# Performance work log

Hardware: AMD Instinct MI355X
Metric: run time of the kernel (lower is better)

The kernel has to match this reference:

```python
import jax, jax.numpy as jnp
import numpy as np

HIDDEN = 1024
HEADS = 16
HEAD_DIM = HIDDEN // HEADS


def setup_inputs() -> dict:
    key = jax.random.key(0)
    ks = jax.random.split(key, 4)
    B, S, H = 2, 2048, HIDDEN
    scale = 1.0 / np.sqrt(H)
    return {
        "inputs": jax.random.normal(ks[0], (B, S, H), dtype=jnp.float32),
        "mask": jnp.ones((B, S), dtype=jnp.int32),
        "Wq": jax.random.normal(ks[1], (H, H), dtype=jnp.float32) * scale,
        "bq": jnp.zeros((H,), dtype=jnp.float32),
        "Wk": jax.random.normal(ks[2], (H, H), dtype=jnp.float32) * scale,
        "bk": jnp.zeros((H,), dtype=jnp.float32),
        "Wv": jax.random.normal(ks[3], (H, H), dtype=jnp.float32) * scale,
        "bv": jnp.zeros((H,), dtype=jnp.float32),
    }


def _split_heads(x, B, S):
    # [B,S,H] -> [B,heads,S,head_dim]
    return x.reshape(B, S, HEADS, HEAD_DIM).transpose(0, 2, 1, 3)


def reference(inputs, mask, Wq, bq, Wk, bk, Wv, bv):
    B, S, H = inputs.shape
    q = _split_heads(inputs @ Wq.T + bq, B, S)
    k = _split_heads(inputs @ Wk.T + bk, B, S)
    v = _split_heads(inputs @ Wv.T + bv, B, S)
    scores = jnp.einsum("bhqd,bhkd->bhqk", q, k) / jnp.sqrt(
        jnp.asarray(HEAD_DIM, dtype=inputs.dtype))
    # mask broadcast [B,1,1,S]; zeros -> -inf
    scores = jnp.where(mask[:, None, None, :] == 0, -jnp.inf, scores)
    attn = jax.nn.softmax(scores, axis=-1)
    context = jnp.einsum("bhqk,bhkd->bhqd", attn, v)
    return context.transpose(0, 2, 1, 3).reshape(B, S, H)
```

## Files before the change

kernel.cpp:

```cpp
#include <hip/hip_runtime.h>
#include <hip/hip_fp16.h>

constexpr int S_LEN  = 2048;
constexpr int HID    = 1024;
constexpr int HEADS  = 16;
constexpr int HDIM   = 64;
constexpr int BATCH  = 2;
constexpr int BH     = BATCH * HEADS;
constexpr int M_ROWS = BATCH * S_LEN;

typedef _Float16 half8  __attribute__((ext_vector_type(8)));
typedef _Float16 half4v __attribute__((ext_vector_type(4)));
typedef _Float16 half2v __attribute__((ext_vector_type(2)));
typedef float    f32x4  __attribute__((ext_vector_type(4)));
typedef float    f32x16 __attribute__((ext_vector_type(16)));

constexpr float EXP2_OFF = -11.541560327111707f;
constexpr float Q_SCALE  = 0.18033688011112042f;

__global__ __launch_bounds__(256) void cvt_kernel(
    const float* __restrict__ X,  const float* __restrict__ Wq,
    const float* __restrict__ Wk, const float* __restrict__ Wv,
    const int* __restrict__ mask,
    _Float16* __restrict__ Xh,  _Float16* __restrict__ Wqh,
    _Float16* __restrict__ Wkh, _Float16* __restrict__ Wvh,
    float* __restrict__ maskF)
{
    const int blk = blockIdx.x;
    if (blk >= 3584) {
        const int loc = blk - 3584;
        const size_t e = ((size_t)loc * 256 + threadIdx.x) * 8;
        #pragma unroll
        for (int i = 0; i < 8; ++i)
            maskF[e + i] = mask[e + i] ? EXP2_OFF : -1.0e30f;
        return;
    }
    const float* src; _Float16* dst; int loc;
    if (blk < 2048)      { src = X;  dst = Xh;  loc = blk; }
    else if (blk < 2560) { src = Wq; dst = Wqh; loc = blk - 2048; }
    else if (blk < 3072) { src = Wk; dst = Wkh; loc = blk - 2560; }
    else                 { src = Wv; dst = Wvh; loc = blk - 3072; }
    const size_t e = ((size_t)loc * 256 + threadIdx.x) * 8;
    float4 a = *reinterpret_cast<const float4*>(&src[e]);
    float4 b = *reinterpret_cast<const float4*>(&src[e + 4]);
    half8 h = { (_Float16)a.x, (_Float16)a.y, (_Float16)a.z, (_Float16)a.w,
                (_Float16)b.x, (_Float16)b.y, (_Float16)b.z, (_Float16)b.w };
    *reinterpret_cast<half8*>(&dst[e]) = h;
}

__device__ __forceinline__ void async_cp16(_Float16* lds, const _Float16* g) {
    __builtin_amdgcn_global_load_lds(
        (const __attribute__((address_space(1))) void*)g,
        (__attribute__((address_space(3))) void*)lds, 16, 0, 0);
}

__global__ __launch_bounds__(256) void qkv_proj_kernel(
    const _Float16* __restrict__ Xh,
    const _Float16* __restrict__ Wqh, const _Float16* __restrict__ Wkh,
    const _Float16* __restrict__ Wvh,
    const float* __restrict__ bq, const float* __restrict__ bk,
    const float* __restrict__ bv,
    _Float16* __restrict__ Qo, _Float16* __restrict__ Ko,
    _Float16* __restrict__ Vt)
{
    const int mode = blockIdx.z;
    const _Float16* W    = (mode == 0) ? Wqh : (mode == 1) ? Wkh : Wvh;
    const float*    bias = (mode == 0) ? bq  : (mode == 1) ? bk  : bv;

    const int m0 = blockIdx.x * 128, n0 = blockIdx.y * 128;
    const int tid = threadIdx.x, wave = tid >> 6, lane = tid & 63;
    const int l31 = lane & 31, kg = lane >> 5;

    __shared__ _Float16 SMEM[18432];

    f32x16 acc[2][2];
    #pragma unroll
    for (int mt = 0; mt < 2; ++mt)
        #pragma unroll
        for (int nt = 0; nt < 2; ++nt)
            #pragma unroll
            for (int i = 0; i < 16; ++i) acc[mt][nt][i] = 0.f;

    const int wm = (wave & 1) * 64, wn = (wave >> 1) * 64;

    const int srow = tid >> 2, spos = tid & 3;
    auto stage = [&](int k0, int b) {
        _Float16* Asb = SMEM + b * 8192;
        _Float16* Bsb = Asb + 4096;
        #pragma unroll
        for (int j = 0; j < 2; ++j) {
            const int row = srow + j * 64;
            const int sch = spos ^ (row & 3);
            async_cp16(&Asb[j * 2048 + tid * 8],
                       &Xh[(size_t)(m0 + row) * HID + k0 + sch * 8]);
            async_cp16(&Bsb[j * 2048 + tid * 8],
                       &W [(size_t)(n0 + row) * HID + k0 + sch * 8]);
        }
    };

    stage(0, 0);
    int buf = 0;

    for (int k0 = 0; k0 < HID; k0 += 32) {
        __syncthreads();
        if (k0 + 32 < HID) stage(k0 + 32, buf ^ 1);
        _Float16* Asb = SMEM + buf * 8192;
        _Float16* Bsb = Asb + 4096;

        #pragma unroll
        for (int c = 0; c < 2; ++c) {
            const int k8 = c * 2 + kg;
            half8 af[2], bf[2];
            #pragma unroll
            for (int mt = 0; mt < 2; ++mt) {
                const int row = wm + mt * 32 + l31;
                af[mt] = *reinterpret_cast<const half8*>(
                    &Asb[row * 32 + ((k8 ^ (row & 3)) * 8)]);
            }
            #pragma unroll
            for (int nt = 0; nt < 2; ++nt) {
                const int row = wn + nt * 32 + l31;
                bf[nt] = *reinterpret_cast<const half8*>(
                    &Bsb[row * 32 + ((k8 ^ (row & 3)) * 8)]);
            }
            #pragma unroll
            for (int mt = 0; mt < 2; ++mt)
                #pragma unroll
                for (int nt = 0; nt < 2; ++nt)
                    acc[mt][nt] = __builtin_amdgcn_mfma_f32_32x32x16_f16(
                        af[mt], bf[nt], acc[mt][nt], 0, 0, 0);
        }
        buf ^= 1;
    }
    __syncthreads();

    _Float16* T = SMEM + wave * 4608;

    const int nn  = n0 + wn;
    const int hh  = nn >> 6;
    const int mm  = m0 + wm;
    const int bb  = mm >> 11;
    const int bhv = bb * HEADS + hh;
    const int s0  = mm & 2047;
    const int rowg = lane >> 3, chunk = lane & 7;

    if (mode < 2) {
        _Float16* Out = (mode == 0) ? Qo : Ko;
        #pragma unroll
        for (int nt = 0; nt < 2; ++nt) {
            const int col = nt * 32 + l31;
            float bias_n = bias[nn + col];
            #pragma unroll
            for (int mt = 0; mt < 2; ++mt)
                #pragma unroll
                for (int r = 0; r < 16; ++r) {
                    const int row_l = (r & 3) + 8 * (r >> 2) + 4 * kg;
                    float v = acc[mt][nt][r] + bias_n;
                    if (mode == 0) v *= Q_SCALE;
                    T[(mt * 32 + row_l) * 72 + col] = (_Float16)v;
                }
        }
        asm volatile("s_waitcnt lgkmcnt(0)" ::: "memory");
        #pragma unroll
        for (int j = 0; j < 8; ++j) {
            const int sr = j * 8 + rowg;
            half8 v = *reinterpret_cast<const half8*>(&T[sr * 72 + chunk * 8]);
            *reinterpret_cast<half8*>(
                &Out[((size_t)bhv * S_LEN + s0 + sr) * HDIM + chunk * 8]) = v;
        }
    } else {
        #pragma unroll
        for (int nt = 0; nt < 2; ++nt) {
            const int col = nt * 32 + l31;
            const float bias_n = bias[nn + col];
            #pragma unroll
            for (int mt = 0; mt < 2; ++mt)
                #pragma unroll
                for (int rg = 0; rg < 4; ++rg) {
                    half4v t = { (_Float16)(acc[mt][nt][rg * 4 + 0] + bias_n),
                                 (_Float16)(acc[mt][nt][rg * 4 + 1] + bias_n),
                                 (_Float16)(acc[mt][nt][rg * 4 + 2] + bias_n),
                                 (_Float16)(acc[mt][nt][rg * 4 + 3] + bias_n) };
                    const int s_off = mt * 32 + 8 * rg + 4 * kg;
                    *reinterpret_cast<half4v*>(&T[col * 72 + s_off]) = t;
                }
        }
        asm volatile("s_waitcnt lgkmcnt(0)" ::: "memory");
        #pragma unroll
        for (int j = 0; j < 8; ++j) {
            const int dr = j * 8 + rowg;
            half8 v = *reinterpret_cast<const half8*>(&T[dr * 72 + chunk * 8]);
            *reinterpret_cast<half8*>(
                &Vt[((size_t)bhv * HDIM + dr) * S_LEN + s0 + chunk * 8]) = v;
        }
    }
}

__global__ __launch_bounds__(512) void attn_kernel(
    const _Float16* __restrict__ Q, const _Float16* __restrict__ K,
    const _Float16* __restrict__ Vt, const float* __restrict__ maskF,
    float* __restrict__ Out)
{
    const int id    = blockIdx.x;
    const int xcd   = id & 7, local = id >> 3;
    const int bh    = xcd * 4 + (local & 3);
    const int qt    = local >> 2;
    const int b = bh >> 4, h = bh & 15;
    const int tid = threadIdx.x, wave = tid >> 6, lane = tid & 63;
    const int l15 = lane & 15, quad = lane >> 4;

    __shared__ _Float16 Ks[2][64 * 64];
    __shared__ _Float16 Vs[2][64 * 64];
    __shared__ _Float16 Ps[8][16][68];

    const _Float16* Qb = Q  + (size_t)bh * S_LEN * HDIM;
    const _Float16* Kb = K  + (size_t)bh * S_LEN * HDIM;
    const _Float16* Vb = Vt + (size_t)bh * HDIM * S_LEN;
    const float*    mb = maskF + b * S_LEN;

    const int qrow = qt * 128 + wave * 16 + l15;
    half8 qf[2];
    qf[0] = *reinterpret_cast<const half8*>(&Qb[(size_t)qrow * HDIM + quad * 8]);
    qf[1] = *reinterpret_cast<const half8*>(&Qb[(size_t)qrow * HDIM + 32 + quad * 8]);

    f32x4 acc[4];
    #pragma unroll
    for (int mt = 0; mt < 4; ++mt) acc[mt] = (f32x4){0.f, 0.f, 0.f, 0.f};
    float den = 0.f;

    const int srow_t  = tid >> 3;
    const int schunk  = (tid & 7) ^ (srow_t & 7);
    auto stage = [&](int kb, int buf) {
        async_cp16(&Ks[buf][tid * 8],
                   &Kb[(size_t)(kb + srow_t) * HDIM + schunk * 8]);
        async_cp16(&Vs[buf][tid * 8],
                   &Vb[(size_t)srow_t * S_LEN + kb + schunk * 8]);
    };

    stage(0, 0);
    int buf = 0;
    const int rsw = (l15 & 7);

    for (int kb = 0; kb < S_LEN; kb += 64) {
        __syncthreads();
        if (kb + 64 < S_LEN) stage(kb + 64, buf ^ 1);

        float4 m4[4];
        #pragma unroll
        for (int nt = 0; nt < 4; ++nt)
            m4[nt] = *reinterpret_cast<const float4*>(&mb[kb + nt * 16 + quad * 4]);

        half8 kf[2][4];
        #pragma unroll
        for (int c = 0; c < 2; ++c)
            #pragma unroll
            for (int nt = 0; nt < 4; ++nt)
                kf[c][nt] = *reinterpret_cast<const half8*>(
                    &Ks[buf][(nt * 16 + l15) * 64 + ((c * 4 + quad) ^ rsw) * 8]);
        f32x4 sc[4];
        #pragma unroll
        for (int nt = 0; nt < 4; ++nt) sc[nt] = (f32x4){0.f, 0.f, 0.f, 0.f};
        #pragma unroll
        for (int c = 0; c < 2; ++c)
            #pragma unroll
            for (int nt = 0; nt < 4; ++nt)
                sc[nt] = __builtin_amdgcn_mfma_f32_16x16x32_f16(
                    kf[c][nt], qf[c], sc[nt], 0, 0, 0);

        half8 vf[2][4];
        #pragma unroll
        for (int c = 0; c < 2; ++c)
            #pragma unroll
            for (int mt = 0; mt < 4; ++mt)
                vf[c][mt] = *reinterpret_cast<const half8*>(
                    &Vs[buf][(mt * 16 + l15) * 64 + ((c * 4 + quad) ^ rsw) * 8]);

        #pragma unroll
        for (int nt = 0; nt < 4; ++nt) {
            float p0 = __builtin_amdgcn_exp2f(sc[nt][0] + m4[nt].x);
            float p1 = __builtin_amdgcn_exp2f(sc[nt][1] + m4[nt].y);
            float p2 = __builtin_amdgcn_exp2f(sc[nt][2] + m4[nt].z);
            float p3 = __builtin_amdgcn_exp2f(sc[nt][3] + m4[nt].w);
            den += (p0 + p1) + (p2 + p3);
            half2v lo = __builtin_bit_cast(half2v, __builtin_amdgcn_cvt_pkrtz(p0, p1));
            half2v hi = __builtin_bit_cast(half2v, __builtin_amdgcn_cvt_pkrtz(p2, p3));
            half4v pk = { lo[0], lo[1], hi[0], hi[1] };
            *reinterpret_cast<half4v*>(&Ps[wave][l15][nt * 16 + quad * 4]) = pk;
        }
        asm volatile("s_waitcnt lgkmcnt(0)" ::: "memory");

        #pragma unroll
        for (int c = 0; c < 2; ++c) {
            half4v plo = *reinterpret_cast<const half4v*>(
                &Ps[wave][l15][c * 32 + quad * 8]);
            half4v phi = *reinterpret_cast<const half4v*>(
                &Ps[wave][l15][c * 32 + quad * 8 + 4]);
            half8 pf = { plo[0], plo[1], plo[2], plo[3],
                         phi[0], phi[1], phi[2], phi[3] };
            #pragma unroll
            for (int mt = 0; mt < 4; ++mt)
                acc[mt] = __builtin_amdgcn_mfma_f32_16x16x32_f16(
                    vf[c][mt], pf, acc[mt], 0, 0, 0);
        }
        buf ^= 1;
    }

    den += __shfl_xor(den, 16, 64);
    den += __shfl_xor(den, 32, 64);
    const float inv = 1.0f / den;

    float* orow = Out + ((size_t)(b * S_LEN + qrow)) * HID + h * HDIM;
    #pragma unroll
    for (int mt = 0; mt < 4; ++mt) {
        float4 o = { acc[mt][0] * inv, acc[mt][1] * inv,
                     acc[mt][2] * inv, acc[mt][3] * inv };
        *reinterpret_cast<float4*>(&orow[mt * 16 + quad * 4]) = o;
    }
}

extern "C" void kernel_launch(void* const* d_in, const int* in_sizes, int n_in,
                              void* d_out, int out_size, void* d_ws, size_t ws_size,
                              hipStream_t stream) {
    const float* X  = (const float*)d_in[0];
    const int*   mk = (const int*)  d_in[1];
    const float* Wq = (const float*)d_in[2];
    const float* bq = (const float*)d_in[3];
    const float* Wk = (const float*)d_in[4];
    const float* bk = (const float*)d_in[5];
    const float* Wv = (const float*)d_in[6];
    const float* bv = (const float*)d_in[7];
    float* out = (float*)d_out;

    _Float16* Xh  = (_Float16*)d_ws;
    _Float16* Wqh = Xh  + (size_t)M_ROWS * HID;
    _Float16* Wkh = Wqh + (size_t)HID * HID;
    _Float16* Wvh = Wkh + (size_t)HID * HID;
    _Float16* Q   = Wvh + (size_t)HID * HID;
    _Float16* K   = Q   + (size_t)BH * S_LEN * HDIM;
    _Float16* Vt  = K   + (size_t)BH * S_LEN * HDIM;
    float*    maskF = (float*)(Vt + (size_t)BH * S_LEN * HDIM);

    cvt_kernel<<<3586, 256, 0, stream>>>(X, Wq, Wk, Wv, mk, Xh, Wqh, Wkh, Wvh, maskF);

    dim3 gp(M_ROWS / 128, HID / 128, 3);
    qkv_proj_kernel<<<gp, 256, 0, stream>>>(Xh, Wqh, Wkh, Wvh, bq, bk, bv, Q, K, Vt);

    attn_kernel<<<512, 512, 0, stream>>>(Q, K, Vt, maskF, out);
}
```

Measured before the change: 173.8 us.

## Process two query groups per wave in attention to reuse K/V fragments

The attention block drops from 8 waves of 16 query rows each to 4 waves of 32 query rows each. Each wave now reuses its K and V fragments loaded from shared memory across two query groups, which halves LDS fragment reads per unit of MFMA work. Staging is split into two copies per thread to fill the same tiles. The cost is more registers per wave for the doubled accumulators and fewer waves per block, which may reduce latency hiding.

After: 175.1 us. Within noise of the previous version (+0.8%).

```diff
diff --git a/kernel.cpp b/kernel.cpp
--- a/kernel.cpp
+++ b/kernel.cpp
@@ -196,7 +196,7 @@
     }
 }
 
-__global__ __launch_bounds__(512) void attn_kernel(
+__global__ __launch_bounds__(256) void attn_kernel(
     const _Float16* __restrict__ Q, const _Float16* __restrict__ K,
     const _Float16* __restrict__ Vt, const float* __restrict__ maskF,
     float* __restrict__ Out)
@@ -211,30 +211,40 @@
 
     __shared__ _Float16 Ks[2][64 * 64];
     __shared__ _Float16 Vs[2][64 * 64];
-    __shared__ _Float16 Ps[8][16][68];
+    __shared__ _Float16 Ps[4][32][68];
 
     const _Float16* Qb = Q  + (size_t)bh * S_LEN * HDIM;
     const _Float16* Kb = K  + (size_t)bh * S_LEN * HDIM;
     const _Float16* Vb = Vt + (size_t)bh * HDIM * S_LEN;
     const float*    mb = maskF + b * S_LEN;
 
-    const int qrow = qt * 128 + wave * 16 + l15;
-    half8 qf[2];
-    qf[0] = *reinterpret_cast<const half8*>(&Qb[(size_t)qrow * HDIM + quad * 8]);
-    qf[1] = *reinterpret_cast<const half8*>(&Qb[(size_t)qrow * HDIM + 32 + quad * 8]);
-
-    f32x4 acc[4];
+    const int qrow0 = qt * 128 + wave * 32 + l15;
+    half8 qf[2][2];
     #pragma unroll
-    for (int mt = 0; mt < 4; ++mt) acc[mt] = (f32x4){0.f, 0.f, 0.f, 0.f};
-    float den = 0.f;
-
-    const int srow_t  = tid >> 3;
-    const int schunk  = (tid & 7) ^ (srow_t & 7);
+    for (int g = 0; g < 2; ++g) {
+        const size_t qo = (size_t)(qrow0 + g * 16) * HDIM;
+        qf[g][0] = *reinterpret_cast<const half8*>(&Qb[qo + quad * 8]);
+        qf[g][1] = *reinterpret_cast<const half8*>(&Qb[qo + 32 + quad * 8]);
+    }
+
+    f32x4 acc[2][4];
+    #pragma unroll
+    for (int g = 0; g < 2; ++g)
+        #pragma unroll
+        for (int mt = 0; mt < 4; ++mt) acc[g][mt] = (f32x4){0.f, 0.f, 0.f, 0.f};
+    float den[2] = {0.f, 0.f};
+
+    const int srow_t = tid >> 3;
+    const int sch    = (tid & 7) ^ (srow_t & 7);
     auto stage = [&](int kb, int buf) {
-        async_cp16(&Ks[buf][tid * 8],
-                   &Kb[(size_t)(kb + srow_t) * HDIM + schunk * 8]);
-        async_cp16(&Vs[buf][tid * 8],
-                   &Vb[(size_t)srow_t * S_LEN + kb + schunk * 8]);
+        #pragma unroll
+        for (int j = 0; j < 2; ++j) {
+            const int row = srow_t + j * 32;
+            async_cp16(&Ks[buf][j * 2048 + tid * 8],
+                       &Kb[(size_t)(kb + row) * HDIM + sch * 8]);
+            async_cp16(&Vs[buf][j * 2048 + tid * 8],
+                       &Vb[(size_t)row * S_LEN + kb + sch * 8]);
+        }
     };
 
     stage(0, 0);
@@ -257,16 +267,6 @@
             for (int nt = 0; nt < 4; ++nt)
                 kf[c][nt] = *reinterpret_cast<const half8*>(
                     &Ks[buf][(nt * 16 + l15) * 64 + ((c * 4 + quad) ^ rsw) * 8]);
-        f32x4 sc[4];
-        #pragma unroll
-        for (int nt = 0; nt < 4; ++nt) sc[nt] = (f32x4){0.f, 0.f, 0.f, 0.f};
-        #pragma unroll
-        for (int c = 0; c < 2; ++c)
-            #pragma unroll
-            for (int nt = 0; nt < 4; ++nt)
-                sc[nt] = __builtin_amdgcn_mfma_f32_16x16x32_f16(
-                    kf[c][nt], qf[c], sc[nt], 0, 0, 0);
-
         half8 vf[2][4];
         #pragma unroll
         for (int c = 0; c < 2; ++c)
@@ -276,45 +276,65 @@
                     &Vs[buf][(mt * 16 + l15) * 64 + ((c * 4 + quad) ^ rsw) * 8]);
 
         #pragma unroll
-        for (int nt = 0; nt < 4; ++nt) {
-            float p0 = __builtin_amdgcn_exp2f(sc[nt][0] + m4[nt].x);
-            float p1 = __builtin_amdgcn_exp2f(sc[nt][1] + m4[nt].y);
-            float p2 = __builtin_amdgcn_exp2f(sc[nt][2] + m4[nt].z);
-            float p3 = __builtin_amdgcn_exp2f(sc[nt][3] + m4[nt].w);
-            den += (p0 + p1) + (p2 + p3);
-            half2v lo = __builtin_bit_cast(half2v, __builtin_amdgcn_cvt_pkrtz(p0, p1));
-            half2v hi = __builtin_bit_cast(half2v, __builtin_amdgcn_cvt_pkrtz(p2, p3));
-            half4v pk = { lo[0], lo[1], hi[0], hi[1] };
-            *reinterpret_cast<half4v*>(&Ps[wave][l15][nt * 16 + quad * 4]) = pk;
+        for (int g = 0; g < 2; ++g) {
+            f32x4 sc[4];
+            #pragma unroll
+            for (int nt = 0; nt < 4; ++nt) sc[nt] = (f32x4){0.f, 0.f, 0.f, 0.f};
+            #pragma unroll
+            for (int c = 0; c < 2; ++c)
+                #pragma unroll
+                for (int nt = 0; nt < 4; ++nt)
+                    sc[nt] = __builtin_amdgcn_mfma_f32_16x16x32_f16(
+                        kf[c][nt], qf[g][c], sc[nt], 0, 0, 0);
+
+            #pragma unroll
+            for (int nt = 0; nt < 4; ++nt) {
+                float p0 = __builtin_amdgcn_exp2f(sc[nt][0] + m4[nt].x);
+                float p1 = __builtin_amdgcn_exp2f(sc[nt][1] + m4[nt].y);
+                float p2 = __builtin_amdgcn_exp2f(sc[nt][2] + m4[nt].z);
+                float p3 = __builtin_amdgcn_exp2f(sc[nt][3] + m4[nt].w);
+                den[g] += (p0 + p1) + (p2 + p3);
+                half2v lo = __builtin_bit_cast(half2v, __builtin_amdgcn_cvt_pkrtz(p0, p1));
+                half2v hi = __builtin_bit_cast(half2v, __builtin_amdgcn_cvt_pkrtz(p2, p3));
+                half4v pk = { lo[0], lo[1], hi[0], hi[1] };
+                *reinterpret_cast<half4v*>(
+                    &Ps[wave][g * 16 + l15][nt * 16 + quad * 4]) = pk;
+            }
         }
         asm volatile("s_waitcnt lgkmcnt(0)" ::: "memory");
 
         #pragma unroll
-        for (int c = 0; c < 2; ++c) {
-            half4v plo = *reinterpret_cast<const half4v*>(
-                &Ps[wave][l15][c * 32 + quad * 8]);
-            half4v phi = *reinterpret_cast<const half4v*>(
-                &Ps[wave][l15][c * 32 + quad * 8 + 4]);
-            half8 pf = { plo[0], plo[1], plo[2], plo[3],
-                         phi[0], phi[1], phi[2], phi[3] };
-            #pragma unroll
-            for (int mt = 0; mt < 4; ++mt)
-                acc[mt] = __builtin_amdgcn_mfma_f32_16x16x32_f16(
-                    vf[c][mt], pf, acc[mt], 0, 0, 0);
+        for (int g = 0; g < 2; ++g) {
+            #pragma unroll
+            for (int c = 0; c < 2; ++c) {
+                half4v plo = *reinterpret_cast<const half4v*>(
+                    &Ps[wave][g * 16 + l15][c * 32 + quad * 8]);
+                half4v phi = *reinterpret_cast<const half4v*>(
+                    &Ps[wave][g * 16 + l15][c * 32 + quad * 8 + 4]);
+                half8 pf = { plo[0], plo[1], plo[2], plo[3],
+                             phi[0], phi[1], phi[2], phi[3] };
+                #pragma unroll
+                for (int mt = 0; mt < 4; ++mt)
+                    acc[g][mt] = __builtin_amdgcn_mfma_f32_16x16x32_f16(
+                        vf[c][mt], pf, acc[g][mt], 0, 0, 0);
+            }
         }
         buf ^= 1;
     }
 
-    den += __shfl_xor(den, 16, 64);
-    den += __shfl_xor(den, 32, 64);
-    const float inv = 1.0f / den;
-
-    float* orow = Out + ((size_t)(b * S_LEN + qrow)) * HID + h * HDIM;
     #pragma unroll
-    for (int mt = 0; mt < 4; ++mt) {
-        float4 o = { acc[mt][0] * inv, acc[mt][1] * inv,
-                     acc[mt][2] * inv, acc[mt][3] * inv };
-        *reinterpret_cast<float4*>(&orow[mt * 16 + quad * 4]) = o;
+    for (int g = 0; g < 2; ++g) {
+        float d = den[g];
+        d += __shfl_xor(d, 16, 64);
+        d += __shfl_xor(d, 32, 64);
+        const float inv = 1.0f / d;
+        float* orow = Out + ((size_t)(b * S_LEN + qrow0 + g * 16)) * HID + h * HDIM;
+        #pragma unroll
+        for (int mt = 0; mt < 4; ++mt) {
+            float4 o = { acc[g][mt][0] * inv, acc[g][mt][1] * inv,
+                         acc[g][mt][2] * inv, acc[g][mt][3] * inv };
+            *reinterpret_cast<float4*>(&orow[mt * 16 + quad * 4]) = o;
+        }
     }
 }
 
@@ -345,5 +365,5 @@
     dim3 gp(M_ROWS / 128, HID / 128, 3);
     qkv_proj_kernel<<<gp, 256, 0, stream>>>(Xh, Wqh, Wkh, Wvh, bq, bk, bv, Q, K, Vt);
 
-    attn_kernel<<<512, 512, 0, stream>>>(Q, K, Vt, maskF, out);
-}
+    attn_kernel<<<512, 256, 0, stream>>>(Q, K, Vt, maskF, out);
+}
```
